# Kernel optimization log

Hardware: AMD Instinct MI355X
Metric: run time of the kernel (lower is better)

The kernel has to match this reference:

```python
import jax, jax.numpy as jnp
import numpy as np

B, L, D, H = 2, 2048, 512, 8
Dh = D // H


def setup_inputs() -> dict:
    key = jax.random.key(0)
    ks = jax.random.split(key, 12)
    def lin(i):
        W = jax.random.normal(ks[i], (D, D), dtype=jnp.float32) * (1.0 / np.sqrt(D))
        b = jax.random.normal(ks[i + 1], (D,), dtype=jnp.float32) * 0.02
        return W, b
    Wq, bq = lin(0)
    Wk, bk = lin(2)
    Wv, bv = lin(4)
    Wo, bo = lin(6)
    wave_real = jax.random.normal(ks[8], (B, L, D), dtype=jnp.float32)
    wave_imag = jax.random.normal(ks[9], (B, L, D), dtype=jnp.float32)
    return {"wave_real": wave_real, "wave_imag": wave_imag,
            "Wq": Wq, "bq": bq, "Wk": Wk, "bk": bk,
            "Wv": Wv, "bv": bv, "Wo": Wo, "bo": bo}


def _heads(x):
    # (B,L,D) -> (B,H,L,Dh)
    return x.reshape(B, L, H, Dh).transpose(0, 2, 1, 3)


def reference(wave_real, wave_imag, Wq, bq, Wk, bk, Wv, bv, Wo, bo):
    Qr = _heads(wave_real @ Wq.T + bq)
    Qi = _heads(wave_imag @ Wq.T + bq)
    Kr = _heads(wave_real @ Wk.T + bk)
    Ki = _heads(wave_imag @ Wk.T + bk)
    Vr = _heads(wave_real @ Wv.T + bv)
    Vi = _heads(wave_imag @ Wv.T + bv)

    inner_real = jnp.einsum('bhid,bhjd->bhij', Qr, Kr) + jnp.einsum('bhid,bhjd->bhij', Qi, Ki)
    inner_imag = jnp.einsum('bhid,bhjd->bhij', Qr, Ki) - jnp.einsum('bhid,bhjd->bhij', Qi, Kr)

    scores = (inner_real ** 2 + inner_imag ** 2) / np.sqrt(Dh).astype(np.float32)
    attention = jax.nn.softmax(scores, axis=-1)

    phase = jnp.arctan2(inner_imag, inner_real)
    ac = attention * jnp.cos(phase)  # (B,H,L,L)
    as_ = attention * jnp.sin(phase)

    # sum_j att_ij*(Vr_j*cos_ij - Vi_j*sin_ij) -- fused contraction, same math as
    # the original's materialized (B,H,L,L,Dh) rotate-then-sum.
    out_real = jnp.einsum('bhij,bhjd->bhid', ac, Vr) - jnp.einsum('bhij,bhjd->bhid', as_, Vi)
    out_imag = jnp.einsum('bhij,bhjd->bhid', as_, Vr) + jnp.einsum('bhij,bhjd->bhid', ac, Vi)

    out_real = out_real.transpose(0, 2, 1, 3).reshape(B, L, D)
    out_imag = out_imag.transpose(0, 2, 1, 3).reshape(B, L, D)
    return (out_real @ Wo.T + bo, out_imag @ Wo.T + bo, attention)
```

## Files before the change

### kernel.cpp

```cpp
#include <hip/hip_runtime.h>

typedef unsigned short u16;
typedef unsigned int   u32;
typedef __attribute__((ext_vector_type(4)))  u16   us4;
typedef __attribute__((ext_vector_type(8)))  u16   us8;
typedef __attribute__((ext_vector_type(8)))  short s8v;
typedef __attribute__((ext_vector_type(16))) float f32x16;

#define L_   2048
#define D_   512
#define H_   8
#define PE_  2097152ull

#define MATE    2097152ull
#define BHE     131072u
#define VT_OFF  33554432ull
#define ORH_OFF 41943040ull
#define ORL_OFF 46137344ull
#define OIH_OFF 50331648ull
#define OIL_OFF 54525952ull
#define LV_OFF  58720256ull

#define XRH_O 16777216ull
#define XRL_O 20971520ull
#define XIH_O 25165824ull
#define XIL_O 29360128ull

#define MFMA32(a,b,c) __builtin_amdgcn_mfma_f32_32x32x16_bf16(a,b,c,0,0,0)
#define ROWOF(r,hi) (((r)&3) + 8*((r)>>2) + 4*(hi))

__device__ __forceinline__ u16 f2bf(float x){
    u32 u = __float_as_uint(x);
    u += 0x7FFFu + ((u>>16)&1u);
    return (u16)(u>>16);
}
__device__ __forceinline__ float bf2f(u16 h){ return __uint_as_float(((u32)h)<<16); }

__device__ __forceinline__ void glds16(const void* gsrc, void* ldst)
{
    __builtin_amdgcn_global_load_lds(
        (const __attribute__((address_space(1))) u32*)(unsigned long long)gsrc,
        (__attribute__((address_space(3))) u32*)(u32)(unsigned long long)ldst,
        16, 0, 0);
}
__device__ __forceinline__ void glds_mat(unsigned char* Lp, u32 matOff,
                                         const u16* g, int rowBase, int lane)
{
    const char* gb = (const char*)(g + (size_t)rowBase * 64);
    #pragma unroll
    for (int s = 0; s < 8; ++s)
        glds16(gb + s*1024 + lane*16, Lp + matOff + s*1024);
}
__device__ __forceinline__ void glds_vt(unsigned char* Lp, u32 matOff,
                                        const u16* g, int j0, int lane, int s0)
{
    #pragma unroll
    for (int s = 0; s < 4; ++s) {
        int seg = s0 + s;
        int dh  = seg*8 + (lane >> 3);
        const char* gp = (const char*)g + (size_t)dh*4096 + (size_t)j0*2 + (lane & 7)*16;
        glds16(gp, Lp + matOff + seg*1024u);
    }
}

__global__ __launch_bounds__(256)
void split_prep_kernel(const float* __restrict__ wr, const float* __restrict__ wi,
                       unsigned char* __restrict__ outb)
{
    const int z = blockIdx.y;
    const float* src = z ? wi : wr;
    u16* hg = (u16*)(outb + (z ? XIH_O : XRH_O));
    u16* lg = (u16*)(outb + (z ? XIL_O : XRL_O));
    const size_t idx4 = ((size_t)blockIdx.x * 256 + threadIdx.x) * 4;
    float4 v = *(const float4*)&src[idx4];
    float vv[4] = { v.x, v.y, v.z, v.w };
    us4 h, l;
    #pragma unroll
    for (int c = 0; c < 4; ++c) {
        u16 hb = f2bf(vv[c]);
        h[c] = hb;
        l[c] = f2bf(vv[c] - bf2f(hb));
    }
    *(us4*)&hg[idx4] = h;
    *(us4*)&lg[idx4] = l;
}

__device__ __forceinline__ s8v ldfrag(const unsigned char* Lp, u32 matOff, u32 row, u32 colb)
{
    return *(const s8v*)(Lp + matOff + row*128u + (colb ^ ((row&7u)<<4)));
}

__global__ __launch_bounds__(256, 2)
void proj_mfma_kernel(const unsigned char* __restrict__ scr,
                      const float* __restrict__ Wq, const float* __restrict__ Wk,
                      const float* __restrict__ Wv,
                      const float* __restrict__ bq, const float* __restrict__ bk,
                      const float* __restrict__ bv,
                      u16* __restrict__ qk, u16* __restrict__ vt)
{
    const int z = blockIdx.z;
    const u16* Ah_g = (const u16*)(scr + ((z & 1) ? XIH_O : XRH_O));
    const u16* Al_g = (const u16*)(scr + ((z & 1) ? XIL_O : XRL_O));
    const int wsel = z >> 1;
    const float* Wf; const float* bias;
    if (wsel == 0)      { Wf = Wq; bias = bq; }
    else if (wsel == 1) { Wf = Wk; bias = bk; }
    else                { Wf = Wv; bias = bv; }
    const bool four = (wsel < 2);

    const int m0 = blockIdx.x * 128;
    const int n0 = blockIdx.y * 64;

    __shared__ __align__(16) unsigned char L[49152];
    enum : u32 { AH=0, AL=16384, BH=32768, BL=40960 };

    const int tid  = threadIdx.x;
    const int lane = tid & 63;
    const int wid  = tid >> 6;
    const int wr   = wid >> 1, wc = wid & 1;
    const int l31  = lane & 31;
    const int hi   = lane >> 5;
    const u32 rowA0 = (u32)(wr*64 + l31);
    const u32 rowB  = (u32)(wc*32 + l31);

    f32x16 c0, c1;
    #pragma unroll
    for (int r = 0; r < 16; ++r) { c0[r] = 0.f; c1[r] = 0.f; }

    const int ch = tid & 7, r0 = tid >> 3;

    for (int k0 = 0; k0 < 512; k0 += 64) {
        __syncthreads();
        #pragma unroll
        for (int rr = 0; rr < 4; ++rr) {
            u32 row = (u32)(rr*32 + r0);
            u32 dst = row*128u + (((u32)ch<<4) ^ ((row&7u)<<4));
            us8 vh = *(const us8*)(Ah_g + (size_t)(m0 + row)*512 + k0 + ch*8);
            *(us8*)(L + AH + dst) = vh;
            if (four) {
                us8 vl = *(const us8*)(Al_g + (size_t)(m0 + row)*512 + k0 + ch*8);
                *(us8*)(L + AL + dst) = vl;
            }
        }
        #pragma unroll
        for (int rr = 0; rr < 2; ++rr) {
            u32 row = (u32)(rr*32 + r0);
            const float* src = Wf + (size_t)(n0 + row)*512 + k0 + ch*8;
            float4 v0 = *(const float4*)src;
            float4 v1 = *(const float4*)(src + 4);
            float vv[8] = { v0.x,v0.y,v0.z,v0.w, v1.x,v1.y,v1.z,v1.w };
            us8 hv, lv;
            #pragma unroll
            for (int j = 0; j < 8; ++j) {
                u16 hb = f2bf(vv[j]);
                hv[j] = hb;
                lv[j] = f2bf(vv[j] - bf2f(hb));
            }
            u32 dst = row*128u + (((u32)ch<<4) ^ ((row&7u)<<4));
            *(us8*)(L + BH + dst) = hv;
            if (four) *(us8*)(L + BL + dst) = lv;
        }
        __syncthreads();

        #pragma unroll
        for (int ks = 0; ks < 4; ++ks) {
            u32 colb = (u32)(ks*32 + hi*16);
            s8v a0h = ldfrag(L, AH, rowA0,      colb);
            s8v a1h = ldfrag(L, AH, rowA0 + 32, colb);
            s8v bh_ = ldfrag(L, BH, rowB,       colb);
            c0 = MFMA32(a0h, bh_, c0);
            c1 = MFMA32(a1h, bh_, c1);
            if (four) {
                s8v a0l = ldfrag(L, AL, rowA0,      colb);
                s8v a1l = ldfrag(L, AL, rowA0 + 32, colb);
                s8v bl_ = ldfrag(L, BL, rowB,       colb);
                c0 = MFMA32(a0h, bl_, c0); c0 = MFMA32(a0l, bh_, c0); c0 = MFMA32(a0l, bl_, c0);
                c1 = MFMA32(a1h, bl_, c1); c1 = MFMA32(a1l, bh_, c1); c1 = MFMA32(a1l, bl_, c1);
            }
        }
    }

    const int n  = n0 + wc*32 + l31;
    const float bvv = bias[n];
    const int h  = n >> 6, dh = n & 63;

    if (z < 4) {
        u16* hg = qk + (size_t)(2*z)   * MATE;
        u16* lg = qk + (size_t)(2*z+1) * MATE;
        #pragma unroll
        for (int f = 0; f < 2; ++f) {
            const f32x16& c = f ? c1 : c0;
            #pragma unroll
            for (int r = 0; r < 16; ++r) {
                int m  = m0 + wr*64 + 32*f + ROWOF(r, hi);
                int b_ = m >> 11, i = m & 2047;
                size_t idx = (size_t)(b_*8 + h)*BHE + (size_t)i*64 + (dh ^ ((i&7)<<3));
                float v = c[r] + bvv;
                u16 hb = f2bf(v);
                hg[idx] = hb;
                lg[idx] = f2bf(v - bf2f(hb));
            }
        }
    } else {
        u16* vg = vt + (size_t)(z & 1) * MATE;
        #pragma unroll
        for (int f = 0; f < 2; ++f) {
            const f32x16& c = f ? c1 : c0;
            #pragma unroll
            for (int g = 0; g < 4; ++g) {
                int mb = m0 + wr*64 + 32*f + 8*g + 4*hi;
                int b_ = mb >> 11, ib = mb & 2047;
                us4 pv;
                #pragma unroll
                for (int j = 0; j < 4; ++j) pv[j] = f2bf(c[4*g + j] + bvv);
                int ibs = ib ^ ((dh & 7) << 3);
                *(us4*)&vg[(size_t)(b_*8 + h)*BHE + (size_t)dh*2048 + ibs] = pv;
            }
        }
    }
}

__global__ __launch_bounds__(256, 2)
void attn_mfma_kernel(const u16* __restrict__ qk,
                      const u16* __restrict__ vt,
                      float* __restrict__ attnbuf,
                      u16* __restrict__ orh, u16* __restrict__ orl,
                      u16* __restrict__ oih, u16* __restrict__ oil,
                      float* __restrict__ l_out)
{
    const int bh = blockIdx.x;
    const int i0 = blockIdx.y * 64;
    const int tid  = threadIdx.x;
    const int lane = tid & 63;
    const int wid  = tid >> 6;
    const int wr   = wid >> 1, wc = wid & 1;
    const int l31  = lane & 31;
    const int hi   = lane >> 5;
    const u32 rowA = wr*32 + l31;
    const u32 rowB = wc*32 + l31;

    __shared__ __align__(16) unsigned char L[81920];
    enum : u32 { QRH=0, QRL=8192, QIH=16384, QIL=24576,
                 KRH=32768, KRL=40960, KIH=49152, KIL=57344,
                 VRo=32768, VIo=40960,
                 PAC=65536, PAS=73728 };
    float* sc = (float*)(L + PAC);

    const u16* qrh = qk + 0*MATE + (size_t)bh*BHE;
    const u16* qrl = qk + 1*MATE + (size_t)bh*BHE;
    const u16* qih = qk + 2*MATE + (size_t)bh*BHE;
    const u16* qil = qk + 3*MATE + (size_t)bh*BHE;
    const u16* krh = qk + 4*MATE + (size_t)bh*BHE;
    const u16* krl = qk + 5*MATE + (size_t)bh*BHE;
    const u16* kih = qk + 6*MATE + (size_t)bh*BHE;
    const u16* kil = qk + 7*MATE + (size_t)bh*BHE;
    const u16* vtr = vt + 0*MATE + (size_t)bh*BHE;
    const u16* vti = vt + 1*MATE + (size_t)bh*BHE;

    {
        const u16* qsrc = (wid == 0) ? qrh : (wid == 1) ? qrl : (wid == 2) ? qih : qil;
        glds_mat(L, (u32)(wid * 8192), qsrc, i0, lane);
    }

    float mxv[16];
    #pragma unroll
    for (int r = 0; r < 16; ++r) mxv[r] = 0.f;

    const u16* s1src = (wid & 1) ? kih : krh;
    const u32  s1off = 32768u + (u32)(wid & 1)*16384u + (u32)(wid >> 1)*8192u;

    for (int jp = 0; jp < 16; ++jp) {
        __syncthreads();
        glds_mat(L, s1off, s1src, (2*jp + (wid >> 1))*64, lane);
        __syncthreads();
        __builtin_amdgcn_s_setprio(1);
        #pragma unroll
        for (int half = 0; half < 2; ++half) {
            const u32 kR = half ? KRL : KRH;
            const u32 kI = half ? KIL : KIH;
            f32x16 ir, ip, in_;
            #pragma unroll
            for (int r = 0; r < 16; ++r) { ir[r]=0.f; ip[r]=0.f; in_[r]=0.f; }
            #pragma unroll
            for (int ks = 0; ks < 4; ++ks) {
                u32 colb = ks*32 + hi*16;
                s8v aR = ldfrag(L, QRH, rowA, colb);
                s8v aI = ldfrag(L, QIH, rowA, colb);
                s8v bR = ldfrag(L, kR,  rowB, colb);
                s8v bI = ldfrag(L, kI,  rowB, colb);
                ir  = MFMA32(aR, bR, ir);
                ir  = MFMA32(aI, bI, ir);
                ip  = MFMA32(aR, bI, ip);
                in_ = MFMA32(aI, bR, in_);
            }
            #pragma unroll
            for (int r = 0; r < 16; ++r) {
                float xr = ir[r], xi = ip[r] - in_[r];
                float q = xr*xr + xi*xi;
                mxv[r] = fmaxf(mxv[r], q * 0.125f);
            }
        }
        __builtin_amdgcn_s_setprio(0);
    }
    #pragma unroll
    for (int m = 1; m < 32; m <<= 1)
        #pragma unroll
        for (int r = 0; r < 16; ++r) mxv[r] = fmaxf(mxv[r], __shfl_xor(mxv[r], m));

    __syncthreads();
    #pragma unroll
    for (int r = 0; r < 16; ++r)
        if (l31 == r) sc[wc*64 + wr*32 + ROWOF(r,hi)] = mxv[r];
    __syncthreads();
    float mfin[16];
    #pragma unroll
    for (int r = 0; r < 16; ++r) {
        u32 row = wr*32 + ROWOF(r,hi);
        mfin[r] = fmaxf(sc[row], sc[64 + row]);
    }

    f32x16 ore, oim;
    float lp[16];
    #pragma unroll
    for (int r = 0; r < 16; ++r) { ore[r]=0.f; oim[r]=0.f; lp[r]=0.f; }

    const u16* s2src = (wid == 0) ? krh : (wid == 1) ? krl : (wid == 2) ? kih : kil;
    const u32  s2off = 32768u + (u32)wid * 8192u;
    const u16* vsrc  = (wid < 2) ? vtr : vti;
    const u32  voff  = (wid < 2) ? VRo : VIo;
    const int  vseg  = (wid & 1) * 4;

    for (int jt = 0; jt < 32; ++jt) {
        const int j0 = jt * 64;
        __syncthreads();
        glds_mat(L, s2off, s2src, j0, lane);
        __syncthreads();

        f32x16 ir, ip, in_;
        #pragma unroll
        for (int r = 0; r < 16; ++r) { ir[r]=0.f; ip[r]=0.f; in_[r]=0.f; }
        __builtin_amdgcn_s_setprio(1);
        #pragma unroll
        for (int ks = 0; ks < 4; ++ks) {
            u32 colb = ks*32 + hi*16;
            s8v aRH = ldfrag(L, QRH, rowA, colb);
            s8v aRL = ldfrag(L, QRL, rowA, colb);
            s8v aIH = ldfrag(L, QIH, rowA, colb);
            s8v aIL = ldfrag(L, QIL, rowA, colb);
            s8v bRH = ldfrag(L, KRH, rowB, colb);
            s8v bRL = ldfrag(L, KRL, rowB, colb);
            s8v bIH = ldfrag(L, KIH, rowB, colb);
            s8v bIL = ldfrag(L, KIL, rowB, colb);
            ir = MFMA32(aRH, bRH, ir); ir = MFMA32(aRH, bRL, ir); ir = MFMA32(aRL, bRH, ir);
            ir = MFMA32(aIH, bIH, ir); ir = MFMA32(aIH, bIL, ir); ir = MFMA32(aIL, bIH, ir);
            ip  = MFMA32(aRH, bIH, ip);  ip  = MFMA32(aRH, bIL, ip);  ip  = MFMA32(aRL, bIH, ip);
            in_ = MFMA32(aIH, bRH, in_); in_ = MFMA32(aIH, bRL, in_); in_ = MFMA32(aIL, bRH, in_);
        }
        __builtin_amdgcn_s_setprio(0);
        __syncthreads();

        glds_vt(L, voff, vsrc, j0, lane, vseg);

        float* arow = attnbuf + (size_t)bh*4194304ull + (size_t)i0*2048 + j0 + wc*32 + l31;
        #pragma unroll
        for (int r = 0; r < 16; ++r) {
            float xr = ir[r], xi = ip[r] - in_[r];
            float q  = fmaf(xr, xr, xi*xi);
            float e  = __expf(fmaf(q, 0.125f, -mfin[r]));
            lp[r] += e;
            float iv = rsqrtf(q);
            float t  = e * iv;
            float pc = (q > 0.f) ? xr*t : e;
            float ps = (q > 0.f) ? xi*t : 0.0f;
            u32 rowloc = wr*32 + ROWOF(r,hi);
            arow[(size_t)rowloc*2048] = e;
            u32 colb2 = (wc*32 + l31)*2;
            *(u16*)(L + PAC + rowloc*128u + (colb2 ^ ((rowloc&7u)<<4))) = f2bf(pc);
            *(u16*)(L + PAS + rowloc*128u + (colb2 ^ ((rowloc&7u)<<4))) = f2bf(ps);
        }
        __syncthreads();

        __builtin_amdgcn_s_setprio(1);
        #pragma unroll
        for (int ks = 0; ks < 4; ++ks) {
            u32 colb = ks*32 + hi*16;
            s8v aC = ldfrag(L, PAC, rowA, colb);
            s8v aS = ldfrag(L, PAS, rowA, colb);
            s8v vR = ldfrag(L, VRo, rowB, colb);
            s8v vI = ldfrag(L, VIo, rowB, colb);
            s8v vN = vI ^ (short)0x8000;
            ore = MFMA32(aC, vR, ore); ore = MFMA32(aS, vN, ore);
            oim = MFMA32(aS, vR, oim); oim = MFMA32(aC, vI, oim);
        }
        __builtin_amdgcn_s_setprio(0);
    }

    #pragma unroll
    for (int m = 1; m < 32; m <<= 1)
        #pragma unroll
        for (int r = 0; r < 16; ++r) lp[r] += __shfl_xor(lp[r], m);

    __syncthreads();
    #pragma unroll
    for (int r = 0; r < 16; ++r)
        if (l31 == r) sc[wc*64 + wr*32 + ROWOF(r,hi)] = lp[r];
    __syncthreads();

    const int b_ = bh >> 3, h = bh & 7;
    const size_t cb = (size_t)h*64 + wc*32 + l31;
    #pragma unroll
    for (int r = 0; r < 16; ++r) {
        u32 row = wr*32 + ROWOF(r,hi);
        float ls = sc[row] + sc[64 + row];
        if (wc == 0 && l31 == 0) l_out[(size_t)bh*2048 + i0 + row] = ls;
        float inv = 1.0f / ls;
        size_t idx = ((size_t)b_*2048 + i0 + row)*512 + cb;
        float vr = ore[r] * inv;
        float vi = oim[r] * inv;
        u16 hr = f2bf(vr); orh[idx] = hr; orl[idx] = f2bf(vr - bf2f(hr));
        u16 hw = f2bf(vi); oih[idx] = hw; oil[idx] = f2bf(vi - bf2f(hw));
    }
}

__global__ __launch_bounds__(256)
void scale_attn_kernel(float* __restrict__ attnbuf, const float* __restrict__ l)
{
    const size_t idx = (size_t)blockIdx.x * 256 + threadIdx.x;
    const size_t row = idx >> 9;
    const float inv = 1.f / l[row];
    float4* p = (float4*)attnbuf + idx;
    float4 v = *p;
    v.x *= inv; v.y *= inv; v.z *= inv; v.w *= inv;
    *p = v;
}

__global__ __launch_bounds__(256, 2)
void oproj_mfma_kernel(const unsigned char* __restrict__ wsb,
                       const float* __restrict__ Wo, const float* __restrict__ bo,
                       float* __restrict__ out)
{
    const int z = blockIdx.z;
    const u16* Ah_g = (const u16*)(wsb + (z ? OIH_OFF : ORH_OFF));
    const u16* Al_g = (const u16*)(wsb + (z ? OIL_OFF : ORL_OFF));
    float* outp = out + (size_t)z * PE_;

    const int m0 = blockIdx.x * 128;
    const int n0 = blockIdx.y * 64;

    __shared__ __align__(16) unsigned char L[49152];
    enum : u32 { AH=0, AL=16384, BH=32768, BL=40960 };

    const int tid  = threadIdx.x;
    const int lane = tid & 63;
    const int wid  = tid >> 6;
    const int wr   = wid >> 1, wc = wid & 1;
    const int l31  = lane & 31;
    const int hi   = lane >> 5;
    const u32 rowA0 = (u32)(wr*64 + l31);
    const u32 rowB  = (u32)(wc*32 + l31);

    f32x16 c0, c1;
    #pragma unroll
    for (int r = 0; r < 16; ++r) { c0[r] = 0.f; c1[r] = 0.f; }

    const int ch = tid & 7, r0 = tid >> 3;

    for (int k0 = 0; k0 < 512; k0 += 64) {
        __syncthreads();
        #pragma unroll
        for (int rr = 0; rr < 4; ++rr) {
            u32 row = (u32)(rr*32 + r0);
            u32 dst = row*128u + (((u32)ch<<4) ^ ((row&7u)<<4));
            us8 vh = *(const us8*)(Ah_g + (size_t)(m0 + row)*512 + k0 + ch*8);
            us8 vl = *(const us8*)(Al_g + (size_t)(m0 + row)*512 + k0 + ch*8);
            *(us8*)(L + AH + dst) = vh;
            *(us8*)(L + AL + dst) = vl;
        }
        #pragma unroll
        for (int rr = 0; rr < 2; ++rr) {
            u32 row = (u32)(rr*32 + r0);
            const float* src = Wo + (size_t)(n0 + row)*512 + k0 + ch*8;
            float4 v0 = *(const float4*)src;
            float4 v1 = *(const float4*)(src + 4);
            float vv[8] = { v0.x,v0.y,v0.z,v0.w, v1.x,v1.y,v1.z,v1.w };
            us8 hv, lv;
            #pragma unroll
            for (int j = 0; j < 8; ++j) {
                u16 hb = f2bf(vv[j]);
                hv[j] = hb;
                lv[j] = f2bf(vv[j] - bf2f(hb));
            }
            u32 dst = row*128u + (((u32)ch<<4) ^ ((row&7u)<<4));
            *(us8*)(L + BH + dst) = hv;
            *(us8*)(L + BL + dst) = lv;
        }
        __syncthreads();

        #pragma unroll
        for (int ks = 0; ks < 4; ++ks) {
            u32 colb = (u32)(ks*32 + hi*16);
            s8v a0h = ldfrag(L, AH, rowA0,      colb);
            s8v a1h = ldfrag(L, AH, rowA0 + 32, colb);
            s8v a0l = ldfrag(L, AL, rowA0,      colb);
            s8v a1l = ldfrag(L, AL, rowA0 + 32, colb);
            s8v bh_ = ldfrag(L, BH, rowB,       colb);
            s8v bl_ = ldfrag(L, BL, rowB,       colb);
            c0 = MFMA32(a0h, bh_, c0); c0 = MFMA32(a0h, bl_, c0); c0 = MFMA32(a0l, bh_, c0);
            c1 = MFMA32(a1h, bh_, c1); c1 = MFMA32(a1h, bl_, c1); c1 = MFMA32(a1l, bh_, c1);
        }
    }

    const int n = n0 + wc*32 + l31;
    const float bvv = bo[n];
    #pragma unroll
    for (int f = 0; f < 2; ++f) {
        const f32x16& c = f ? c1 : c0;
        #pragma unroll
        for (int r = 0; r < 16; ++r) {
            int m = m0 + wr*64 + 32*f + ROWOF(r, hi);
            outp[(size_t)m*512 + n] = c[r] + bvv;
        }
    }
}

extern "C" void kernel_launch(void* const* d_in, const int* in_sizes, int n_in,
                              void* d_out, int out_size, void* d_ws, size_t ws_size,
                              hipStream_t stream)
{
    const float* wave_real = (const float*)d_in[0];
    const float* wave_imag = (const float*)d_in[1];
    const float* Wq = (const float*)d_in[2]; const float* bq = (const float*)d_in[3];
    const float* Wk = (const float*)d_in[4]; const float* bk = (const float*)d_in[5];
    const float* Wv = (const float*)d_in[6]; const float* bv = (const float*)d_in[7];
    const float* Wo = (const float*)d_in[8]; const float* bo = (const float*)d_in[9];
    float* out = (float*)d_out;
    unsigned char* outb = (unsigned char*)d_out;
    unsigned char* wsb  = (unsigned char*)d_ws;

    float* attnbuf = out + 2*PE_;

    split_prep_kernel<<<dim3(2048, 2), dim3(256), 0, stream>>>(wave_real, wave_imag, outb);

    proj_mfma_kernel<<<dim3(32, 8, 6), dim3(256), 0, stream>>>(
        outb, Wq, Wk, Wv, bq, bk, bv,
        (u16*)wsb, (u16*)(wsb + VT_OFF));

    attn_mfma_kernel<<<dim3(16, 32), dim3(256), 0, stream>>>(
        (const u16*)wsb, (const u16*)(wsb + VT_OFF), attnbuf,
        (u16*)(wsb + ORH_OFF), (u16*)(wsb + ORL_OFF),
        (u16*)(wsb + OIH_OFF), (u16*)(wsb + OIL_OFF),
        (float*)(wsb + LV_OFF));

    scale_attn_kernel<<<dim3(65536), dim3(256), 0, stream>>>(
        attnbuf, (const float*)(wsb + LV_OFF));

    oproj_mfma_kernel<<<dim3(32, 8, 2), dim3(256), 0, stream>>>(
        wsb, Wo, bo, out);
}
```

Baseline: 364.6 us.

## Hold Q low parts in registers, co-load V with K, fuse scale into oproj

```diff
diff --git a/kernel.cpp b/kernel.cpp
--- a/kernel.cpp
+++ b/kernel.cpp
@@ -240,9 +240,9 @@
     const u32 rowB = wc*32 + l31;
 
     __shared__ __align__(16) unsigned char L[81920];
-    enum : u32 { QRH=0, QRL=8192, QIH=16384, QIL=24576,
-                 KRH=32768, KRL=40960, KIH=49152, KIL=57344,
-                 VRo=32768, VIo=40960,
+    enum : u32 { QRH=0, QIH=8192,
+                 KRH=16384, KRL=24576, KIH=32768, KIL=40960,
+                 VRo=49152, VIo=57344,
                  PAC=65536, PAS=73728 };
     float* sc = (float*)(L + PAC);
 
@@ -258,8 +258,17 @@
     const u16* vti = vt + 1*MATE + (size_t)bh*BHE;
 
     {
-        const u16* qsrc = (wid == 0) ? qrh : (wid == 1) ? qrl : (wid == 2) ? qih : qil;
-        glds_mat(L, (u32)(wid * 8192), qsrc, i0, lane);
+        const u16* qsrc = (wid == 0) ? qrh : (wid == 1) ? qih : (wid == 2) ? qrl : qil;
+        const u32  qdst = (wid == 0) ? QRH : (wid == 1) ? QIH : (wid == 2) ? KRH : KRL;
+        glds_mat(L, qdst, qsrc, i0, lane);
+    }
+    __syncthreads();
+    s8v qfl[2][4];
+    #pragma unroll
+    for (int ks = 0; ks < 4; ++ks) {
+        u32 colb = (u32)(ks*32 + hi*16);
+        qfl[0][ks] = ldfrag(L, KRH, rowA, colb);
+        qfl[1][ks] = ldfrag(L, KRL, rowA, colb);
     }
 
     float mxv[16];
@@ -267,7 +276,7 @@
     for (int r = 0; r < 16; ++r) mxv[r] = 0.f;
 
     const u16* s1src = (wid & 1) ? kih : krh;
-    const u32  s1off = 32768u + (u32)(wid & 1)*16384u + (u32)(wid >> 1)*8192u;
+    const u32  s1off = 16384u + (u32)wid * 8192u;
 
     for (int jp = 0; jp < 16; ++jp) {
         __syncthreads();
@@ -276,8 +285,8 @@
         __builtin_amdgcn_s_setprio(1);
         #pragma unroll
         for (int half = 0; half < 2; ++half) {
-            const u32 kR = half ? KRL : KRH;
-            const u32 kI = half ? KIL : KIH;
+            const u32 kR = half ? KIH : KRH;
+            const u32 kI = half ? KIL : KRL;
             f32x16 ir, ip, in_;
             #pragma unroll
             for (int r = 0; r < 16; ++r) { ir[r]=0.f; ip[r]=0.f; in_[r]=0.f; }
@@ -325,7 +334,7 @@
     for (int r = 0; r < 16; ++r) { ore[r]=0.f; oim[r]=0.f; lp[r]=0.f; }
 
     const u16* s2src = (wid == 0) ? krh : (wid == 1) ? krl : (wid == 2) ? kih : kil;
-    const u32  s2off = 32768u + (u32)wid * 8192u;
+    const u32  s2off = 16384u + (u32)wid * 8192u;
     const u16* vsrc  = (wid < 2) ? vtr : vti;
     const u32  voff  = (wid < 2) ? VRo : VIo;
     const int  vseg  = (wid & 1) * 4;
@@ -334,6 +343,7 @@
         const int j0 = jt * 64;
         __syncthreads();
         glds_mat(L, s2off, s2src, j0, lane);
+        glds_vt(L, voff, vsrc, j0, lane, vseg);
         __syncthreads();
 
         f32x16 ir, ip, in_;
@@ -344,9 +354,9 @@
         for (int ks = 0; ks < 4; ++ks) {
             u32 colb = ks*32 + hi*16;
             s8v aRH = ldfrag(L, QRH, rowA, colb);
-            s8v aRL = ldfrag(L, QRL, rowA, colb);
             s8v aIH = ldfrag(L, QIH, rowA, colb);
-            s8v aIL = ldfrag(L, QIL, rowA, colb);
+            s8v aRL = qfl[0][ks];
+            s8v aIL = qfl[1][ks];
             s8v bRH = ldfrag(L, KRH, rowB, colb);
             s8v bRL = ldfrag(L, KRL, rowB, colb);
             s8v bIH = ldfrag(L, KIH, rowB, colb);
@@ -357,9 +367,6 @@
             in_ = MFMA32(aIH, bRH, in_); in_ = MFMA32(aIH, bRL, in_); in_ = MFMA32(aIL, bRH, in_);
         }
         __builtin_amdgcn_s_setprio(0);
-        __syncthreads();
-
-        glds_vt(L, voff, vsrc, j0, lane, vseg);
 
         float* arow = attnbuf + (size_t)bh*4194304ull + (size_t)i0*2048 + j0 + wc*32 + l31;
         #pragma unroll
@@ -422,33 +429,36 @@
     }
 }
 
-__global__ __launch_bounds__(256)
-void scale_attn_kernel(float* __restrict__ attnbuf, const float* __restrict__ l)
-{
-    const size_t idx = (size_t)blockIdx.x * 256 + threadIdx.x;
-    const size_t row = idx >> 9;
-    const float inv = 1.f / l[row];
-    float4* p = (float4*)attnbuf + idx;
-    float4 v = *p;
-    v.x *= inv; v.y *= inv; v.z *= inv; v.w *= inv;
-    *p = v;
-}
-
 __global__ __launch_bounds__(256, 2)
-void oproj_mfma_kernel(const unsigned char* __restrict__ wsb,
-                       const float* __restrict__ Wo, const float* __restrict__ bo,
-                       float* __restrict__ out)
-{
-    const int z = blockIdx.z;
+void tail_kernel(const unsigned char* __restrict__ wsb,
+                 const float* __restrict__ Wo, const float* __restrict__ bo,
+                 float* __restrict__ out,
+                 float* __restrict__ attnbuf, const float* __restrict__ lv)
+{
+    __shared__ __align__(16) unsigned char L[49152];
+    enum : u32 { AH=0, AL=16384, BH=32768, BL=40960 };
+
+    const int bid = blockIdx.x;
+    if (bid >= 512) {
+        const size_t idx = (size_t)(bid - 512) * 256 + threadIdx.x;
+        const size_t row = idx >> 9;
+        const float inv = 1.f / lv[row];
+        float4* p = (float4*)attnbuf + idx;
+        float4 v = *p;
+        v.x *= inv; v.y *= inv; v.z *= inv; v.w *= inv;
+        *p = v;
+        return;
+    }
+
+    const int z  = bid >> 8;
+    const int bx = bid & 31;
+    const int by = (bid >> 5) & 7;
     const u16* Ah_g = (const u16*)(wsb + (z ? OIH_OFF : ORH_OFF));
     const u16* Al_g = (const u16*)(wsb + (z ? OIL_OFF : ORL_OFF));
     float* outp = out + (size_t)z * PE_;
 
-    const int m0 = blockIdx.x * 128;
-    const int n0 = blockIdx.y * 64;
-
-    __shared__ __align__(16) unsigned char L[49152];
-    enum : u32 { AH=0, AL=16384, BH=32768, BL=40960 };
+    const int m0 = bx * 128;
+    const int n0 = by * 64;
 
     const int tid  = threadIdx.x;
     const int lane = tid & 63;
@@ -483,16 +493,16 @@
             float4 v0 = *(const float4*)src;
             float4 v1 = *(const float4*)(src + 4);
             float vv[8] = { v0.x,v0.y,v0.z,v0.w, v1.x,v1.y,v1.z,v1.w };
-            us8 hv, lv;
+            us8 hv, lv2;
             #pragma unroll
             for (int j = 0; j < 8; ++j) {
                 u16 hb = f2bf(vv[j]);
                 hv[j] = hb;
-                lv[j] = f2bf(vv[j] - bf2f(hb));
+                lv2[j] = f2bf(vv[j] - bf2f(hb));
             }
             u32 dst = row*128u + (((u32)ch<<4) ^ ((row&7u)<<4));
             *(us8*)(L + BH + dst) = hv;
-            *(us8*)(L + BL + dst) = lv;
+            *(us8*)(L + BL + dst) = lv2;
         }
         __syncthreads();
 
@@ -551,9 +561,6 @@
         (u16*)(wsb + OIH_OFF), (u16*)(wsb + OIL_OFF),
         (float*)(wsb + LV_OFF));
 
-    scale_attn_kernel<<<dim3(65536), dim3(256), 0, stream>>>(
-        attnbuf, (const float*)(wsb + LV_OFF));
-
-    oproj_mfma_kernel<<<dim3(32, 8, 2), dim3(256), 0, stream>>>(
-        wsb, Wo, bo, out);
-}
+    tail_kernel<<<dim3(66048), dim3(256), 0, stream>>>(
+        wsb, Wo, bo, out, attnbuf, (const float*)(wsb + LV_OFF));
+}
```

Measured after the change: 387.8 us. 6.4% more time.
